# Kernel optimization log

Hardware: AMD Instinct MI355X
Metric: run time of the kernel (lower is better)

Reference implementation:

```python
import jax, jax.numpy as jnp
import numpy as np

DIM = 768
NUM_HEADS = 16
HEAD_DIM = DIM // NUM_HEADS
SCALE = HEAD_DIM ** -0.5


def setup_inputs() -> dict:
    key = jax.random.key(0)
    ks = jax.random.split(key, 5)
    B, S = 2, 2048
    x = jax.random.normal(ks[0], (B, S, DIM), dtype=jnp.float32)
    # nn.Linear(dim, dim, bias=False): weight shape [out, in]; y = x @ W.T
    init = 1.0 / np.sqrt(DIM)
    Wq = jax.random.uniform(ks[1], (DIM, DIM), jnp.float32, -init, init)
    Wk = jax.random.uniform(ks[2], (DIM, DIM), jnp.float32, -init, init)
    Wv = jax.random.uniform(ks[3], (DIM, DIM), jnp.float32, -init, init)
    Wo = jax.random.uniform(ks[4], (DIM, DIM), jnp.float32, -init, init)
    return {"x": x, "Wq": Wq, "Wk": Wk, "Wv": Wv, "Wo": Wo}


def reference(x, Wq, Wk, Wv, Wo):
    B, S, _ = x.shape
    # projections (torch Linear: x @ W.T)
    q = jnp.einsum('bsd,ed->bse', x, Wq).reshape(B, S, NUM_HEADS, HEAD_DIM)
    k = jnp.einsum('bsd,ed->bse', x, Wk).reshape(B, S, NUM_HEADS, HEAD_DIM)
    v = jnp.einsum('bsd,ed->bse', x, Wv).reshape(B, S, NUM_HEADS, HEAD_DIM)
    # [B, H, S, S] scores, stable softmax, then context
    scores = jnp.einsum('bqhd,bkhd->bhqk', q, k) * SCALE
    probs = jax.nn.softmax(scores, axis=-1)  # dropout is identity in eval
    ctx = jnp.einsum('bhqk,bkhd->bqhd', probs, v).reshape(B, S, DIM)
    return jnp.einsum('bsd,ed->bse', ctx, Wo)
```

## Files before the change

kernel.cpp:

```cpp
#include <hip/hip_runtime.h>
#include <cstdint>

#define DIM 768
#define SEQ 2048
#define NB 2
#define NH 16
#define HD 48
#define NROWS (NB*SEQ)

typedef __attribute__((ext_vector_type(8))) short bf16x8;
typedef __attribute__((ext_vector_type(4))) float f32x4;
typedef __attribute__((ext_vector_type(16))) float f32x16;
typedef unsigned int u32;

__device__ __forceinline__ short f2bf(float f) {
    union { float f; uint32_t u; } v; v.f = f;
    uint32_t u = v.u;
    uint32_t r = (u + 0x7FFFu + ((u >> 16) & 1u)) >> 16;
    return (short)r;
}

__global__ __launch_bounds__(256)
void cvt_bf16(const float* __restrict__ x,  const float* __restrict__ wq,
              const float* __restrict__ wk, const float* __restrict__ wv,
              const float* __restrict__ wo, short* __restrict__ dst)
{
    const int XN4 = (NROWS*DIM)/4;
    const int WN4 = (DIM*DIM)/4;
    const int T4  = XN4 + 4*WN4;
    for (int i = blockIdx.x*blockDim.x + threadIdx.x; i < T4; i += gridDim.x*blockDim.x) {
        const float* src; int off;
        if (i < XN4) { src = x; off = i; }
        else {
            int j = i - XN4;
            int w = j / WN4, r = j - w*WN4;
            src = (w==0) ? wq : (w==1) ? wk : (w==2) ? wv : wo;
            off = r;
        }
        float4 v = *(const float4*)(src + (size_t)off*4);
        short4 s; s.x=f2bf(v.x); s.y=f2bf(v.y); s.z=f2bf(v.z); s.w=f2bf(v.w);
        *(short4*)(dst + (size_t)i*4) = s;
    }
}

template<bool F32OUT>
__global__ __launch_bounds__(256)
void gemm_mfma(const short* __restrict__ A,
               const short* __restrict__ B0, const short* __restrict__ B1,
               const short* __restrict__ B2,
               void* __restrict__ C0v, void* __restrict__ C1v, void* __restrict__ C2v)
{
    const short* B = B0; void* Cv = C0v;
    if (blockIdx.z == 1) { B = B1; Cv = C1v; }
    else if (blockIdx.z == 2) { B = B2; Cv = C2v; }

    __shared__ short As[128*64];
    __shared__ short Bs[128*64];

    const int tid  = threadIdx.x;
    const int lane = tid & 63;
    const int wid  = tid >> 6;
    const int wr = wid >> 1, wc = wid & 1;
    const int m  = lane & 15, kb = lane >> 4;
    const int m0 = blockIdx.y * 128, n0 = blockIdx.x * 128;

    f32x4 acc[4][4];
#pragma unroll
    for (int i = 0; i < 4; ++i)
#pragma unroll
        for (int j = 0; j < 4; ++j) acc[i][j] = (f32x4){0.f,0.f,0.f,0.f};

    for (int k0 = 0; k0 < DIM; k0 += 64) {
        bf16x8 a_st[4], b_st[4];
#pragma unroll
        for (int i = 0; i < 4; ++i) {
            int c = tid + i*256;
            int row = c >> 3, slot = c & 7;
            int gs = slot ^ (row & 7);
            a_st[i] = *(const bf16x8*)&A[(size_t)(m0+row)*DIM + k0 + gs*8];
            b_st[i] = *(const bf16x8*)&B[(size_t)(n0+row)*DIM + k0 + gs*8];
        }
        __syncthreads();
#pragma unroll
        for (int i = 0; i < 4; ++i) {
            int c = tid + i*256;
            int row = c >> 3, slot = c & 7;
            *(bf16x8*)&As[row*64 + slot*8] = a_st[i];
            *(bf16x8*)&Bs[row*64 + slot*8] = b_st[i];
        }
        __syncthreads();

        bf16x8 af[2][4], bfr[2][4];
#pragma unroll
        for (int t = 0; t < 2; ++t) {
            int sl = ((t*4 + kb) ^ (m & 7)) * 8;
#pragma unroll
            for (int f = 0; f < 4; ++f) {
                af[t][f]  = *(const bf16x8*)&As[(wr*64 + f*16 + m)*64 + sl];
                bfr[t][f] = *(const bf16x8*)&Bs[(wc*64 + f*16 + m)*64 + sl];
            }
        }
#pragma unroll
        for (int fm = 0; fm < 4; ++fm)
#pragma unroll
            for (int fn = 0; fn < 4; ++fn) {
                acc[fm][fn] = __builtin_amdgcn_mfma_f32_16x16x32_bf16(af[0][fm], bfr[0][fn], acc[fm][fn], 0, 0, 0);
                acc[fm][fn] = __builtin_amdgcn_mfma_f32_16x16x32_bf16(af[1][fm], bfr[1][fn], acc[fm][fn], 0, 0, 0);
            }
    }

#pragma unroll
    for (int fm = 0; fm < 4; ++fm)
#pragma unroll
        for (int fn = 0; fn < 4; ++fn) {
            int col = n0 + wc*64 + fn*16 + m;
#pragma unroll
            for (int r = 0; r < 4; ++r) {
                int row = m0 + wr*64 + fm*16 + kb*4 + r;
                if (F32OUT)
                    ((float*)Cv)[(size_t)row*DIM + col] = acc[fm][fn][r];
                else
                    ((short*)Cv)[(size_t)row*DIM + col] = f2bf(acc[fm][fn][r]);
            }
        }
}

__global__ __launch_bounds__(256)
void flash2(const short* __restrict__ Qb, const short* __restrict__ Kb,
            const short* __restrict__ Vb, short* __restrict__ Ctx)
{
    __shared__ short K_lds[64*64];
    __shared__ short Vt_lds[64*68];

    const int tid  = threadIdx.x;
    const int wid  = tid >> 6, lane = tid & 63;
    const int r    = lane & 31, hi = lane >> 5;
    const size_t base = (size_t)blockIdx.z*SEQ*DIM + (size_t)blockIdx.y*HD;
    const int q0 = blockIdx.x*128 + wid*32;
    const float C2  = 0.20823688f;
    const float THR = 11.5f;

    for (int i = tid; i < 16*68; i += 256) Vt_lds[48*68 + i] = 0;

    bf16x8 qf[3];
#pragma unroll
    for (int s = 0; s < 3; ++s)
        qf[s] = *(const bf16x8*)&Qb[base + (size_t)(q0 + r)*DIM + s*16 + hi*8];

    f32x16 z16;
#pragma unroll
    for (int i = 0; i < 16; ++i) z16[i] = 0.f;

    f32x16 acc0 = z16, acc1 = z16;
    float m_i = -1e30f, l_i = 0.f;

    const int row0 = tid >> 3,       ps0 = tid & 7;
    const int row1 = (tid+256) >> 3, ps1 = tid & 7;
    const int ls0 = ps0 ^ (row0 & 7), ls1 = ps1 ^ (row1 & 7);

    bf16x8 k0r, k1r; short vreg[12];
    k0r = *(const bf16x8*)&Kb[base + (size_t)row0*DIM + ls0*8];
    k1r = *(const bf16x8*)&Kb[base + (size_t)row1*DIM + ls1*8];
#pragma unroll
    for (int j = 0; j < 12; ++j)
        vreg[j] = Vb[base + (size_t)lane*DIM + wid*12 + j];

    for (int t = 0; t < SEQ/64; ++t) {
        __syncthreads();
        *(bf16x8*)&K_lds[row0*64 + ps0*8] = k0r;
        *(bf16x8*)&K_lds[row1*64 + ps1*8] = k1r;
#pragma unroll
        for (int j = 0; j < 12; ++j)
            Vt_lds[(wid*12 + j)*68 + lane] = vreg[j];
        __syncthreads();

        if (t + 1 < SEQ/64) {
            int c0 = (t+1)*64;
            k0r = *(const bf16x8*)&Kb[base + (size_t)(c0 + row0)*DIM + ls0*8];
            k1r = *(const bf16x8*)&Kb[base + (size_t)(c0 + row1)*DIM + ls1*8];
#pragma unroll
            for (int j = 0; j < 12; ++j)
                vreg[j] = Vb[base + (size_t)(c0 + lane)*DIM + wid*12 + j];
        }

        f32x16 sa[2];
#pragma unroll
        for (int ct = 0; ct < 2; ++ct) {
            f32x16 a = z16;
#pragma unroll
            for (int s = 0; s < 3; ++s) {
                int row = ct*32 + r;
                bf16x8 kf = *(const bf16x8*)&K_lds[row*64 + ((s*2+hi) ^ (row&7))*8];
                a = __builtin_amdgcn_mfma_f32_32x32x16_bf16(kf, qf[s], a, 0, 0, 0);
            }
            sa[ct] = a;
        }

        float mx = -1e30f;
#pragma unroll
        for (int ct = 0; ct < 2; ++ct)
#pragma unroll
            for (int i = 0; i < 16; ++i) mx = fmaxf(mx, sa[ct][i]);
        mx = fmaxf(mx, __shfl_xor(mx, 32));
        mx *= C2;

        float mn = m_i;
        if (!__all(mx - m_i <= THR)) {
            mn = fmaxf(m_i, mx);
            float al = exp2f(m_i - mn);
            l_i *= al;
#pragma unroll
            for (int i = 0; i < 16; ++i) { acc0[i] *= al; acc1[i] *= al; }
            m_i = mn;
        }

        float rs = 0.f;
        u32 w[2][8], sw[2][8];
#pragma unroll
        for (int ct = 0; ct < 2; ++ct)
#pragma unroll
            for (int k = 0; k < 8; ++k) {
                float p0 = exp2f(fmaf(sa[ct][2*k],   C2, -mn));
                float p1 = exp2f(fmaf(sa[ct][2*k+1], C2, -mn));
                u32 b0 = __float_as_uint(p0), b1 = __float_as_uint(p1);
                w[ct][k] = (b1 & 0xffff0000u) | (b0 >> 16);
                rs += __uint_as_float(b0 & 0xffff0000u) + __uint_as_float(b1 & 0xffff0000u);
            }
        rs += __shfl_xor(rs, 32);
        l_i += rs;
#pragma unroll
        for (int ct = 0; ct < 2; ++ct)
#pragma unroll
            for (int k = 0; k < 8; ++k) sw[ct][k] = (u32)__shfl_xor((int)w[ct][k], 32);

#pragma unroll
        for (int ct = 0; ct < 2; ++ct)
#pragma unroll
            for (int hf = 0; hf < 2; ++hf) {
                u32 f0 = hi ? sw[ct][4*hf+2] : w[ct][4*hf+0];
                u32 f1 = hi ? sw[ct][4*hf+3] : w[ct][4*hf+1];
                u32 f2 = hi ? w[ct][4*hf+2]  : sw[ct][4*hf+0];
                u32 f3 = hi ? w[ct][4*hf+3]  : sw[ct][4*hf+1];
                int4 pw = make_int4((int)f0, (int)f1, (int)f2, (int)f3);
                bf16x8 pb = __builtin_bit_cast(bf16x8, pw);
#pragma unroll
                for (int dt = 0; dt < 2; ++dt) {
                    int off = (dt*32 + r)*68 + ct*32 + hf*16 + hi*8;
                    short4 v0 = *(const short4*)&Vt_lds[off];
                    short4 v1 = *(const short4*)&Vt_lds[off + 4];
                    bf16x8 av = {v0.x, v0.y, v0.z, v0.w, v1.x, v1.y, v1.z, v1.w};
                    if (dt == 0) acc0 = __builtin_amdgcn_mfma_f32_32x32x16_bf16(av, pb, acc0, 0, 0, 0);
                    else         acc1 = __builtin_amdgcn_mfma_f32_32x32x16_bf16(av, pb, acc1, 0, 0, 0);
                }
            }
    }

    float inv = 1.0f / l_i;
#pragma unroll
    for (int g = 0; g < 16; ++g) {
        int d = (g&3) + 8*(g>>2) + 4*hi;
        Ctx[base + (size_t)(q0 + r)*DIM + d] = f2bf(acc0[g] * inv);
    }
#pragma unroll
    for (int g = 0; g < 8; ++g) {
        int d = 32 + (g&3) + 8*(g>>2) + 4*hi;
        Ctx[base + (size_t)(q0 + r)*DIM + d] = f2bf(acc1[g] * inv);
    }
}

extern "C" void kernel_launch(void* const* d_in, const int* in_sizes, int n_in,
                              void* d_out, int out_size, void* d_ws, size_t ws_size,
                              hipStream_t stream)
{
    const float* x  = (const float*)d_in[0];
    const float* Wq = (const float*)d_in[1];
    const float* Wk = (const float*)d_in[2];
    const float* Wv = (const float*)d_in[3];
    const float* Wo = (const float*)d_in[4];
    float* out = (float*)d_out;

    const size_t XN = (size_t)NROWS * DIM;
    const size_t WN = (size_t)DIM * DIM;

    short* xb   = (short*)d_ws;
    short* wqb  = xb  + XN;
    short* wkb  = wqb + WN;
    short* wvb  = wkb + WN;
    short* wob  = wvb + WN;
    short* qb   = wob + WN;
    short* kbuf = qb  + XN;
    short* vbuf = kbuf + XN;
    short* ctxb = vbuf + XN;

    cvt_bf16<<<1024, 256, 0, stream>>>(x, Wq, Wk, Wv, Wo, xb);

    dim3 g1(DIM/128, NROWS/128, 3);
    gemm_mfma<false><<<g1, 256, 0, stream>>>(xb, wqb, wkb, wvb, qb, kbuf, vbuf);

    dim3 g2(SEQ/128, NH, NB);
    flash2<<<g2, 256, 0, stream>>>(qb, kbuf, vbuf, ctxb);

    dim3 g3(DIM/128, NROWS/128, 1);
    gemm_mfma<true><<<g3, 256, 0, stream>>>(ctxb, wob, wob, wob, out, out, out);
}
```

Baseline: 195.9 us.

## Fuse fp32-to-bf16 conversion into GEMMs, use 96-wide tiles and register prefetch

Removes the separate conversion kernel and the bf16 staging copies of x and weights. The GEMMs now load fp32 directly and pack to bf16 with the hardware v_cvt_pk_bf16_f32 instruction. The N tile shrinks from 128 to 96 so the grid has more blocks, and the next k-tile is prefetched into registers while the current one is computed. The flash kernel also uses the packed convert for P and sums unrounded probabilities, which slightly changes rounding. The cost is twice the global read bytes for A and B in each GEMM, and the weights are re-converted by every block.

```diff
diff --git a/kernel.cpp b/kernel.cpp
--- a/kernel.cpp
+++ b/kernel.cpp
@@ -20,104 +20,117 @@
     return (short)r;
 }
 
+__device__ __forceinline__ u32 cvtpk(float lo, float hi) {
+    u32 r;
+    asm("v_cvt_pk_bf16_f32 %0, %1, %2" : "=v"(r) : "v"(lo), "v"(hi));
+    return r;
+}
+__device__ __forceinline__ bf16x8 pack8(float4 a, float4 b) {
+    int4 w = make_int4((int)cvtpk(a.x, a.y), (int)cvtpk(a.z, a.w),
+                       (int)cvtpk(b.x, b.y), (int)cvtpk(b.z, b.w));
+    return __builtin_bit_cast(bf16x8, w);
+}
+
+template<bool A_F32, bool OUT_F32>
 __global__ __launch_bounds__(256)
-void cvt_bf16(const float* __restrict__ x,  const float* __restrict__ wq,
-              const float* __restrict__ wk, const float* __restrict__ wv,
-              const float* __restrict__ wo, short* __restrict__ dst)
+void gemm96(const void* __restrict__ Av,
+            const float* __restrict__ B0, const float* __restrict__ B1,
+            const float* __restrict__ B2,
+            void* __restrict__ C0v, void* __restrict__ C1v, void* __restrict__ C2v)
 {
-    const int XN4 = (NROWS*DIM)/4;
-    const int WN4 = (DIM*DIM)/4;
-    const int T4  = XN4 + 4*WN4;
-    for (int i = blockIdx.x*blockDim.x + threadIdx.x; i < T4; i += gridDim.x*blockDim.x) {
-        const float* src; int off;
-        if (i < XN4) { src = x; off = i; }
-        else {
-            int j = i - XN4;
-            int w = j / WN4, r = j - w*WN4;
-            src = (w==0) ? wq : (w==1) ? wk : (w==2) ? wv : wo;
-            off = r;
-        }
-        float4 v = *(const float4*)(src + (size_t)off*4);
-        short4 s; s.x=f2bf(v.x); s.y=f2bf(v.y); s.z=f2bf(v.z); s.w=f2bf(v.w);
-        *(short4*)(dst + (size_t)i*4) = s;
-    }
-}
-
-template<bool F32OUT>
-__global__ __launch_bounds__(256)
-void gemm_mfma(const short* __restrict__ A,
-               const short* __restrict__ B0, const short* __restrict__ B1,
-               const short* __restrict__ B2,
-               void* __restrict__ C0v, void* __restrict__ C1v, void* __restrict__ C2v)
-{
-    const short* B = B0; void* Cv = C0v;
+    const float* B = B0; void* Cv = C0v;
     if (blockIdx.z == 1) { B = B1; Cv = C1v; }
     else if (blockIdx.z == 2) { B = B2; Cv = C2v; }
 
     __shared__ short As[128*64];
-    __shared__ short Bs[128*64];
+    __shared__ short Bs[96*64];
 
     const int tid  = threadIdx.x;
     const int lane = tid & 63;
     const int wid  = tid >> 6;
     const int wr = wid >> 1, wc = wid & 1;
     const int m  = lane & 15, kb = lane >> 4;
-    const int m0 = blockIdx.y * 128, n0 = blockIdx.x * 128;
-
-    f32x4 acc[4][4];
+    const int m0 = blockIdx.y * 128, n0 = blockIdx.x * 96;
+
+    f32x4 acc[4][3];
 #pragma unroll
     for (int i = 0; i < 4; ++i)
 #pragma unroll
-        for (int j = 0; j < 4; ++j) acc[i][j] = (f32x4){0.f,0.f,0.f,0.f};
-
-    for (int k0 = 0; k0 < DIM; k0 += 64) {
-        bf16x8 a_st[4], b_st[4];
+        for (int j = 0; j < 3; ++j) acc[i][j] = (f32x4){0.f,0.f,0.f,0.f};
+
+    bf16x8 sa[4], sb[3];
+
+#define LOAD_A(k0, i) {                                                       \
+        int c = tid + (i)*256; int row = c >> 3, gs = (c & 7) ^ (row & 7);    \
+        if (A_F32) {                                                          \
+            const float* p = (const float*)Av + (size_t)(m0+row)*DIM + (k0) + gs*8; \
+            sa[i] = pack8(*(const float4*)p, *(const float4*)(p+4));          \
+        } else {                                                              \
+            sa[i] = *(const bf16x8*)((const short*)Av + (size_t)(m0+row)*DIM + (k0) + gs*8); \
+        } }
+#define LOAD_B(k0, i) {                                                       \
+        int c = tid + (i)*256; int row = c >> 3, gs = (c & 7) ^ (row & 7);    \
+        const float* p = B + (size_t)(n0+row)*DIM + (k0) + gs*8;              \
+        sb[i] = pack8(*(const float4*)p, *(const float4*)(p+4)); }
+
+#pragma unroll
+    for (int i = 0; i < 4; ++i) LOAD_A(0, i);
+#pragma unroll
+    for (int i = 0; i < 3; ++i) LOAD_B(0, i);
+
+    for (int kt = 0; kt < DIM/64; ++kt) {
+        __syncthreads();
 #pragma unroll
         for (int i = 0; i < 4; ++i) {
             int c = tid + i*256;
-            int row = c >> 3, slot = c & 7;
-            int gs = slot ^ (row & 7);
-            a_st[i] = *(const bf16x8*)&A[(size_t)(m0+row)*DIM + k0 + gs*8];
-            b_st[i] = *(const bf16x8*)&B[(size_t)(n0+row)*DIM + k0 + gs*8];
+            *(bf16x8*)&As[(c>>3)*64 + (c&7)*8] = sa[i];
+        }
+#pragma unroll
+        for (int i = 0; i < 3; ++i) {
+            int c = tid + i*256;
+            *(bf16x8*)&Bs[(c>>3)*64 + (c&7)*8] = sb[i];
         }
         __syncthreads();
-#pragma unroll
-        for (int i = 0; i < 4; ++i) {
-            int c = tid + i*256;
-            int row = c >> 3, slot = c & 7;
-            *(bf16x8*)&As[row*64 + slot*8] = a_st[i];
-            *(bf16x8*)&Bs[row*64 + slot*8] = b_st[i];
-        }
-        __syncthreads();
-
-        bf16x8 af[2][4], bfr[2][4];
+
+        if (kt < DIM/64 - 1) {
+            int k0 = (kt+1)*64;
+#pragma unroll
+            for (int i = 0; i < 4; ++i) LOAD_A(k0, i);
+#pragma unroll
+            for (int i = 0; i < 3; ++i) LOAD_B(k0, i);
+        }
+
+        bf16x8 af[2][4], bfr[2][3];
 #pragma unroll
         for (int t = 0; t < 2; ++t) {
             int sl = ((t*4 + kb) ^ (m & 7)) * 8;
 #pragma unroll
-            for (int f = 0; f < 4; ++f) {
+            for (int f = 0; f < 4; ++f)
                 af[t][f]  = *(const bf16x8*)&As[(wr*64 + f*16 + m)*64 + sl];
-                bfr[t][f] = *(const bf16x8*)&Bs[(wc*64 + f*16 + m)*64 + sl];
-            }
+#pragma unroll
+            for (int f = 0; f < 3; ++f)
+                bfr[t][f] = *(const bf16x8*)&Bs[(wc*48 + f*16 + m)*64 + sl];
         }
 #pragma unroll
         for (int fm = 0; fm < 4; ++fm)
 #pragma unroll
-            for (int fn = 0; fn < 4; ++fn) {
+            for (int fn = 0; fn < 3; ++fn) {
                 acc[fm][fn] = __builtin_amdgcn_mfma_f32_16x16x32_bf16(af[0][fm], bfr[0][fn], acc[fm][fn], 0, 0, 0);
                 acc[fm][fn] = __builtin_amdgcn_mfma_f32_16x16x32_bf16(af[1][fm], bfr[1][fn], acc[fm][fn], 0, 0, 0);
             }
     }
+#undef LOAD_A
+#undef LOAD_B
 
 #pragma unroll
     for (int fm = 0; fm < 4; ++fm)
 #pragma unroll
-        for (int fn = 0; fn < 4; ++fn) {
-            int col = n0 + wc*64 + fn*16 + m;
+        for (int fn = 0; fn < 3; ++fn) {
+            int col = n0 + wc*48 + fn*16 + m;
 #pragma unroll
             for (int r = 0; r < 4; ++r) {
                 int row = m0 + wr*64 + fm*16 + kb*4 + r;
-                if (F32OUT)
+                if (OUT_F32)
                     ((float*)Cv)[(size_t)row*DIM + col] = acc[fm][fn][r];
                 else
                     ((short*)Cv)[(size_t)row*DIM + col] = f2bf(acc[fm][fn][r]);
@@ -222,9 +235,8 @@
             for (int k = 0; k < 8; ++k) {
                 float p0 = exp2f(fmaf(sa[ct][2*k],   C2, -mn));
                 float p1 = exp2f(fmaf(sa[ct][2*k+1], C2, -mn));
-                u32 b0 = __float_as_uint(p0), b1 = __float_as_uint(p1);
-                w[ct][k] = (b1 & 0xffff0000u) | (b0 >> 16);
-                rs += __uint_as_float(b0 & 0xffff0000u) + __uint_as_float(b1 & 0xffff0000u);
+                w[ct][k] = cvtpk(p0, p1);
+                rs += p0 + p1;
             }
         rs += __shfl_xor(rs, 32);
         l_i += rs;
@@ -280,26 +292,18 @@
     float* out = (float*)d_out;
 
     const size_t XN = (size_t)NROWS * DIM;
-    const size_t WN = (size_t)DIM * DIM;
-
-    short* xb   = (short*)d_ws;
-    short* wqb  = xb  + XN;
-    short* wkb  = wqb + WN;
-    short* wvb  = wkb + WN;
-    short* wob  = wvb + WN;
-    short* qb   = wob + WN;
-    short* kbuf = qb  + XN;
+
+    short* qb   = (short*)d_ws;
+    short* kbuf = qb   + XN;
     short* vbuf = kbuf + XN;
     short* ctxb = vbuf + XN;
 
-    cvt_bf16<<<1024, 256, 0, stream>>>(x, Wq, Wk, Wv, Wo, xb);
-
-    dim3 g1(DIM/128, NROWS/128, 3);
-    gemm_mfma<false><<<g1, 256, 0, stream>>>(xb, wqb, wkb, wvb, qb, kbuf, vbuf);
+    dim3 g1(DIM/96, NROWS/128, 3);
+    gemm96<true, false><<<g1, 256, 0, stream>>>(x, Wq, Wk, Wv, qb, kbuf, vbuf);
 
     dim3 g2(SEQ/128, NH, NB);
     flash2<<<g2, 256, 0, stream>>>(qb, kbuf, vbuf, ctxb);
 
-    dim3 g3(DIM/128, NROWS/128, 1);
-    gemm_mfma<true><<<g3, 256, 0, stream>>>(ctxb, wob, wob, wob, out, out, out);
-}
+    dim3 g3(DIM/96, NROWS/128, 1);
+    gemm96<false, true><<<g3, 256, 0, stream>>>(ctxb, Wo, Wo, Wo, out, out, out);
+}
```

New measurement: 196.5 us. Within noise of the previous version (+0.3%).

## Fuse QKV into one strided GEMM with direct-to-LDS loads and 96-wide tiles

Applied to the files above, without the earlier changes.

Writes Q, K and V into a single interleaved buffer of row stride 2304 using one GEMM over the concatenated weights. The GEMM loads tiles with global_load_lds, which bypasses registers, and drops the XOR swizzle. N tiles shrink from 128 to 96 so more blocks exist. Flash attention now reads Q/K/V through the new stride and packs probabilities with the hardware v_cvt_pk_bf16_f32 instruction. Without the swizzle, LDS reads may hit bank conflicts, and the row sum now uses unrounded fp32 values instead of truncated ones.

```diff
diff --git a/kernel.cpp b/kernel.cpp
--- a/kernel.cpp
+++ b/kernel.cpp
@@ -7,6 +7,7 @@
 #define NH 16
 #define HD 48
 #define NROWS (NB*SEQ)
+#define QSTR 2304
 
 typedef __attribute__((ext_vector_type(8))) short bf16x8;
 typedef __attribute__((ext_vector_type(4))) float f32x4;
@@ -18,6 +19,17 @@
     uint32_t u = v.u;
     uint32_t r = (u + 0x7FFFu + ((u >> 16) & 1u)) >> 16;
     return (short)r;
+}
+__device__ __forceinline__ u32 cvtpk(float lo, float hi) {
+    u32 r;
+    asm("v_cvt_pk_bf16_f32 %0, %1, %2" : "=v"(r) : "v"(lo), "v"(hi));
+    return r;
+}
+
+__device__ __forceinline__ void gload16(const short* g, short* l) {
+    __builtin_amdgcn_global_load_lds(
+        (const __attribute__((address_space(1))) void*)g,
+        (__attribute__((address_space(3))) void*)l, 16, 0, 0);
 }
 
 __global__ __launch_bounds__(256)
@@ -43,67 +55,58 @@
     }
 }
 
-template<bool F32OUT>
+template<bool OUT_F32>
 __global__ __launch_bounds__(256)
-void gemm_mfma(const short* __restrict__ A,
-               const short* __restrict__ B0, const short* __restrict__ B1,
-               const short* __restrict__ B2,
-               void* __restrict__ C0v, void* __restrict__ C1v, void* __restrict__ C2v)
+void gemm_gl(const short* __restrict__ A, const short* __restrict__ B,
+             void* __restrict__ Cv, int CN)
 {
-    const short* B = B0; void* Cv = C0v;
-    if (blockIdx.z == 1) { B = B1; Cv = C1v; }
-    else if (blockIdx.z == 2) { B = B2; Cv = C2v; }
-
     __shared__ short As[128*64];
-    __shared__ short Bs[128*64];
+    __shared__ short Bs[96*64];
 
     const int tid  = threadIdx.x;
     const int lane = tid & 63;
     const int wid  = tid >> 6;
     const int wr = wid >> 1, wc = wid & 1;
     const int m  = lane & 15, kb = lane >> 4;
-    const int m0 = blockIdx.y * 128, n0 = blockIdx.x * 128;
-
-    f32x4 acc[4][4];
+    const int m0 = blockIdx.y * 128, n0 = blockIdx.x * 96;
+    const int lr = lane >> 3, lsl = lane & 7;
+
+    f32x4 acc[4][3];
 #pragma unroll
     for (int i = 0; i < 4; ++i)
 #pragma unroll
-        for (int j = 0; j < 4; ++j) acc[i][j] = (f32x4){0.f,0.f,0.f,0.f};
-
-    for (int k0 = 0; k0 < DIM; k0 += 64) {
-        bf16x8 a_st[4], b_st[4];
+        for (int j = 0; j < 3; ++j) acc[i][j] = (f32x4){0.f,0.f,0.f,0.f};
+
+    for (int kt = 0; kt < DIM/64; ++kt) {
+        const int k0 = kt * 64;
+        __syncthreads();
 #pragma unroll
         for (int i = 0; i < 4; ++i) {
-            int c = tid + i*256;
-            int row = c >> 3, slot = c & 7;
-            int gs = slot ^ (row & 7);
-            a_st[i] = *(const bf16x8*)&A[(size_t)(m0+row)*DIM + k0 + gs*8];
-            b_st[i] = *(const bf16x8*)&B[(size_t)(n0+row)*DIM + k0 + gs*8];
+            int r0 = wid*32 + i*8;
+            gload16(&A[(size_t)(m0 + r0 + lr)*DIM + k0 + lsl*8], &As[r0*64]);
+        }
+#pragma unroll
+        for (int i = 0; i < 3; ++i) {
+            int r0 = wid*24 + i*8;
+            gload16(&B[(size_t)(n0 + r0 + lr)*DIM + k0 + lsl*8], &Bs[r0*64]);
         }
         __syncthreads();
-#pragma unroll
-        for (int i = 0; i < 4; ++i) {
-            int c = tid + i*256;
-            int row = c >> 3, slot = c & 7;
-            *(bf16x8*)&As[row*64 + slot*8] = a_st[i];
-            *(bf16x8*)&Bs[row*64 + slot*8] = b_st[i];
-        }
-        __syncthreads();
-
-        bf16x8 af[2][4], bfr[2][4];
+
+        bf16x8 af[2][4], bfr[2][3];
 #pragma unroll
         for (int t = 0; t < 2; ++t) {
-            int sl = ((t*4 + kb) ^ (m & 7)) * 8;
-#pragma unroll
-            for (int f = 0; f < 4; ++f) {
+            int sl = (t*4 + kb) * 8;
+#pragma unroll
+            for (int f = 0; f < 4; ++f)
                 af[t][f]  = *(const bf16x8*)&As[(wr*64 + f*16 + m)*64 + sl];
-                bfr[t][f] = *(const bf16x8*)&Bs[(wc*64 + f*16 + m)*64 + sl];
-            }
+#pragma unroll
+            for (int f = 0; f < 3; ++f)
+                bfr[t][f] = *(const bf16x8*)&Bs[(wc*48 + f*16 + m)*64 + sl];
         }
 #pragma unroll
         for (int fm = 0; fm < 4; ++fm)
 #pragma unroll
-            for (int fn = 0; fn < 4; ++fn) {
+            for (int fn = 0; fn < 3; ++fn) {
                 acc[fm][fn] = __builtin_amdgcn_mfma_f32_16x16x32_bf16(af[0][fm], bfr[0][fn], acc[fm][fn], 0, 0, 0);
                 acc[fm][fn] = __builtin_amdgcn_mfma_f32_16x16x32_bf16(af[1][fm], bfr[1][fn], acc[fm][fn], 0, 0, 0);
             }
@@ -112,15 +115,15 @@
 #pragma unroll
     for (int fm = 0; fm < 4; ++fm)
 #pragma unroll
-        for (int fn = 0; fn < 4; ++fn) {
-            int col = n0 + wc*64 + fn*16 + m;
+        for (int fn = 0; fn < 3; ++fn) {
+            int col = n0 + wc*48 + fn*16 + m;
 #pragma unroll
             for (int r = 0; r < 4; ++r) {
                 int row = m0 + wr*64 + fm*16 + kb*4 + r;
-                if (F32OUT)
-                    ((float*)Cv)[(size_t)row*DIM + col] = acc[fm][fn][r];
+                if (OUT_F32)
+                    ((float*)Cv)[(size_t)row*CN + col] = acc[fm][fn][r];
                 else
-                    ((short*)Cv)[(size_t)row*DIM + col] = f2bf(acc[fm][fn][r]);
+                    ((short*)Cv)[(size_t)row*CN + col] = f2bf(acc[fm][fn][r]);
             }
         }
 }
@@ -135,7 +138,8 @@
     const int tid  = threadIdx.x;
     const int wid  = tid >> 6, lane = tid & 63;
     const int r    = lane & 31, hi = lane >> 5;
-    const size_t base = (size_t)blockIdx.z*SEQ*DIM + (size_t)blockIdx.y*HD;
+    const size_t base  = (size_t)blockIdx.z*SEQ*QSTR + (size_t)blockIdx.y*HD;
+    const size_t baseC = (size_t)blockIdx.z*SEQ*DIM  + (size_t)blockIdx.y*HD;
     const int q0 = blockIdx.x*128 + wid*32;
     const float C2  = 0.20823688f;
     const float THR = 11.5f;
@@ -145,7 +149,7 @@
     bf16x8 qf[3];
 #pragma unroll
     for (int s = 0; s < 3; ++s)
-        qf[s] = *(const bf16x8*)&Qb[base + (size_t)(q0 + r)*DIM + s*16 + hi*8];
+        qf[s] = *(const bf16x8*)&Qb[base + (size_t)(q0 + r)*QSTR + s*16 + hi*8];
 
     f32x16 z16;
 #pragma unroll
@@ -159,11 +163,11 @@
     const int ls0 = ps0 ^ (row0 & 7), ls1 = ps1 ^ (row1 & 7);
 
     bf16x8 k0r, k1r; short vreg[12];
-    k0r = *(const bf16x8*)&Kb[base + (size_t)row0*DIM + ls0*8];
-    k1r = *(const bf16x8*)&Kb[base + (size_t)row1*DIM + ls1*8];
+    k0r = *(const bf16x8*)&Kb[base + (size_t)row0*QSTR + ls0*8];
+    k1r = *(const bf16x8*)&Kb[base + (size_t)row1*QSTR + ls1*8];
 #pragma unroll
     for (int j = 0; j < 12; ++j)
-        vreg[j] = Vb[base + (size_t)lane*DIM + wid*12 + j];
+        vreg[j] = Vb[base + (size_t)lane*QSTR + wid*12 + j];
 
     for (int t = 0; t < SEQ/64; ++t) {
         __syncthreads();
@@ -176,11 +180,11 @@
 
         if (t + 1 < SEQ/64) {
             int c0 = (t+1)*64;
-            k0r = *(const bf16x8*)&Kb[base + (size_t)(c0 + row0)*DIM + ls0*8];
-            k1r = *(const bf16x8*)&Kb[base + (size_t)(c0 + row1)*DIM + ls1*8];
+            k0r = *(const bf16x8*)&Kb[base + (size_t)(c0 + row0)*QSTR + ls0*8];
+            k1r = *(const bf16x8*)&Kb[base + (size_t)(c0 + row1)*QSTR + ls1*8];
 #pragma unroll
             for (int j = 0; j < 12; ++j)
-                vreg[j] = Vb[base + (size_t)(c0 + lane)*DIM + wid*12 + j];
+                vreg[j] = Vb[base + (size_t)(c0 + lane)*QSTR + wid*12 + j];
         }
 
         f32x16 sa[2];
@@ -222,9 +226,8 @@
             for (int k = 0; k < 8; ++k) {
                 float p0 = exp2f(fmaf(sa[ct][2*k],   C2, -mn));
                 float p1 = exp2f(fmaf(sa[ct][2*k+1], C2, -mn));
-                u32 b0 = __float_as_uint(p0), b1 = __float_as_uint(p1);
-                w[ct][k] = (b1 & 0xffff0000u) | (b0 >> 16);
-                rs += __uint_as_float(b0 & 0xffff0000u) + __uint_as_float(b1 & 0xffff0000u);
+                w[ct][k] = cvtpk(p0, p1);
+                rs += p0 + p1;
             }
         rs += __shfl_xor(rs, 32);
         l_i += rs;
@@ -259,12 +262,12 @@
 #pragma unroll
     for (int g = 0; g < 16; ++g) {
         int d = (g&3) + 8*(g>>2) + 4*hi;
-        Ctx[base + (size_t)(q0 + r)*DIM + d] = f2bf(acc0[g] * inv);
+        Ctx[baseC + (size_t)(q0 + r)*DIM + d] = f2bf(acc0[g] * inv);
     }
 #pragma unroll
     for (int g = 0; g < 8; ++g) {
         int d = 32 + (g&3) + 8*(g>>2) + 4*hi;
-        Ctx[base + (size_t)(q0 + r)*DIM + d] = f2bf(acc1[g] * inv);
+        Ctx[baseC + (size_t)(q0 + r)*DIM + d] = f2bf(acc1[g] * inv);
     }
 }
 
@@ -283,23 +286,19 @@
     const size_t WN = (size_t)DIM * DIM;
 
     short* xb   = (short*)d_ws;
-    short* wqb  = xb  + XN;
-    short* wkb  = wqb + WN;
-    short* wvb  = wkb + WN;
-    short* wob  = wvb + WN;
-    short* qb   = wob + WN;
-    short* kbuf = qb  + XN;
-    short* vbuf = kbuf + XN;
-    short* ctxb = vbuf + XN;
+    short* wcat = xb   + XN;
+    short* wob  = wcat + 3*WN;
+    short* qkv  = wob  + WN;
+    short* ctxb = qkv  + (size_t)NROWS*QSTR;
 
     cvt_bf16<<<1024, 256, 0, stream>>>(x, Wq, Wk, Wv, Wo, xb);
 
-    dim3 g1(DIM/128, NROWS/128, 3);
-    gemm_mfma<false><<<g1, 256, 0, stream>>>(xb, wqb, wkb, wvb, qb, kbuf, vbuf);
+    dim3 g1(QSTR/96, NROWS/128, 1);
+    gemm_gl<false><<<g1, 256, 0, stream>>>(xb, wcat, qkv, QSTR);
 
     dim3 g2(SEQ/128, NH, NB);
-    flash2<<<g2, 256, 0, stream>>>(qb, kbuf, vbuf, ctxb);
-
-    dim3 g3(DIM/128, NROWS/128, 1);
-    gemm_mfma<true><<<g3, 256, 0, stream>>>(ctxb, wob, wob, wob, out, out, out);
-}
+    flash2<<<g2, 256, 0, stream>>>(qkv, qkv + DIM, qkv + 2*DIM, ctxb);
+
+    dim3 g3(DIM/96, NROWS/128, 1);
+    gemm_gl<true><<<g3, 256, 0, stream>>>(ctxb, wob, out, DIM);
+}
```

After: 194.3 us. Within noise of the previous version (-0.8%).
